# Optimization experiments

Measured on AMD Instinct MI355X. Metric: run time of the kernel, lower is better.

The kernel has to match this reference:

```python
import jax, jax.numpy as jnp
import numpy as np


def setup_inputs() -> dict:
    key = jax.random.key(0)
    ks = jax.random.split(key, 12)
    B, Nv, C, H, W = 4, 4096, 64, 376, 1240
    inp = {
        "voxel_features": jax.random.normal(ks[0], (B, Nv, C), jnp.float32),
        "voxels_3d": jax.random.normal(ks[1], (B, Nv, 3), jnp.float32),
        "img_feats": jax.random.normal(ks[2], (B, C, H, W), jnp.float32),
        "vox_x": jax.random.randint(ks[3], (B, Nv), 0, 1400, jnp.int32),
        "vox_y": jax.random.randint(ks[4], (B, Nv), 0, 430, jnp.int32),
        "q_w": jax.random.normal(ks[5], (C, C), jnp.float32) / np.sqrt(C),
        "q_b": jnp.zeros((C,), jnp.float32),
        "k_w": jax.random.normal(ks[6], (C, 3), jnp.float32) / np.sqrt(3.0),
        "k_b": jnp.zeros((C,), jnp.float32),
        "v_w": jax.random.normal(ks[7], (C, C), jnp.float32) / np.sqrt(C),
        "v_b": jnp.zeros((C,), jnp.float32),
        "o_w": jax.random.normal(ks[8], (C, C), jnp.float32) / np.sqrt(C),
        "o_b": jnp.zeros((C,), jnp.float32),
        "fc_w": jax.random.normal(ks[9], (C, C), jnp.float32) / np.sqrt(C),
    }
    return inp


def reference(voxel_features, voxels_3d, img_feats, vox_x, vox_y,
              q_w, q_b, k_w, k_b, v_w, v_b, o_w, o_b, fc_w):
    # voxel_features: [B, Nv, C] lidar voxel features (value)
    # voxels_3d:      [B, Nv, 3] voxel 3D coords (key)
    # img_feats:      [B, C, H, W] image feature map
    B, C, H, W = img_feats.shape
    Nv = voxel_features.shape[1]

    # --- gather image features at projected voxel pixel coords, zero if OOB ---
    valid = (vox_x >= 0) & (vox_x < W) & (vox_y >= 0) & (vox_y < H)  # [B, Nv]
    xc = jnp.clip(vox_x, 0, W - 1)
    yc = jnp.clip(vox_y, 0, H - 1)
    b_idx = jnp.arange(B)[:, None]
    camera = img_feats[b_idx, :, yc, xc]            # [B, Nv, C]
    camera = jnp.where(valid[..., None], camera, 0.0)

    # --- single-head cross-modal attention (q=camera, k=coords, v=lidar) ---
    scale = 1.0 / jnp.sqrt(jnp.asarray(C, camera.dtype))
    q = (camera @ q_w.T + q_b) * scale              # [B, Nv, C]
    k = voxels_3d @ k_w.T + k_b                     # [B, Nv, C]
    v = voxel_features @ v_w.T + v_b                # [B, Nv, C]
    scores = jnp.einsum('bqc,bkc->bqk', q, k)       # [B, Nv, Nv]
    attn = jax.nn.softmax(scores, axis=-1)
    ctx = jnp.einsum('bqk,bkc->bqc', attn, v)
    ctx = ctx @ o_w.T + o_b                         # out_proj

    fused = jax.nn.relu(ctx @ fc_w.T)               # [B, Nv, C]
    return jnp.concatenate([voxel_features, fused], axis=-1)  # [B, Nv, 2C]
```

## Files before the change

kernel.cpp:

```cpp
#include <hip/hip_runtime.h>

#define BB 4
#define NV 4096
#define BN (BB * NV)
#define CC 64
#define HH 376
#define WW 1240
#define HW (HH * WW)
#define LDT 72
#define LDK 36
#define NSPLIT 4
#define TILES 16
#define QSCALE 0.1803368801111244f

typedef __bf16 bf16x8 __attribute__((ext_vector_type(8)));
typedef __bf16 bf16x4 __attribute__((ext_vector_type(4)));
typedef float  f32x4  __attribute__((ext_vector_type(4)));

__global__ __launch_bounds__(256) void kprep(
    const float* __restrict__ vfeat, const float* __restrict__ v3d,
    const float* __restrict__ img, const int* __restrict__ vx,
    const int* __restrict__ vy, const float* __restrict__ qw,
    const float* __restrict__ qb, const float* __restrict__ kwm,
    const float* __restrict__ vw, const float* __restrict__ vb,
    float* __restrict__ out, unsigned short* __restrict__ Qp,
    unsigned short* __restrict__ K32, unsigned short* __restrict__ VTb) {
  __shared__ float VfS[32][68];
  __shared__ float CamS[32][68];
  __shared__ float WqkS[64][4];
  __shared__ float bqkS[4];
  const int tid = threadIdx.x;
  const int vl = tid >> 3;
  const int p = tid & 7;
  const int gv = blockIdx.x * 32 + vl;
  const int b = gv >> 12, n = gv & (NV - 1);
  const size_t row = (size_t)b * NV + n;

  if (tid < 192) {
    int j = tid / 3, d = tid - j * 3;
    float a = 0.f;
    for (int c = 0; c < CC; ++c) a = fmaf(qw[c * CC + j], kwm[c * 3 + d], a);
    WqkS[j][d] = a;
  } else if (tid < 195) {
    int d = tid - 192;
    float a = 0.f;
    for (int c = 0; c < CC; ++c) a = fmaf(qb[c], kwm[c * 3 + d], a);
    bqkS[d] = a;
  }

  {
    const float4* vf4 = (const float4*)(vfeat + row * CC) + p * 2;
    float4* o4 = (float4*)(out + row * 128) + p * 2;
    float4* s4 = (float4*)&VfS[vl][p * 8];
#pragma unroll
    for (int i = 0; i < 2; ++i) { float4 t = vf4[i]; o4[i] = t; s4[i] = t; }
  }

  {
    int x = vx[row], y = vy[row];
    bool valid = (x >= 0) & (x < WW) & (y >= 0) & (y < HH);
    int xs = valid ? x : 0, ys = valid ? y : 0;
    const float* ib = img + ((size_t)b * CC + p * 8) * (size_t)HW + (size_t)ys * WW + xs;
#pragma unroll
    for (int i = 0; i < 8; ++i) {
      float cv = ib[(size_t)i * HW];
      CamS[vl][p * 8 + i] = valid ? cv : 0.f;
    }
  }

  if (p == 0) {
    float c0 = v3d[row * 3 + 0], c1 = v3d[row * 3 + 1], c2 = v3d[row * 3 + 2];
    bf16x8 kp = {(__bf16)c0, (__bf16)c1, (__bf16)c2, (__bf16)0.f,
                 (__bf16)0.f, (__bf16)0.f, (__bf16)0.f, (__bf16)0.f};
    *(bf16x8*)(K32 + row * 32) = kp;
  } else if (p < 4) {
    bf16x8 z = {(__bf16)0.f, (__bf16)0.f, (__bf16)0.f, (__bf16)0.f,
                (__bf16)0.f, (__bf16)0.f, (__bf16)0.f, (__bf16)0.f};
    *(bf16x8*)(K32 + row * 32 + p * 8) = z;
  }
  __syncthreads();

  {
    f32x4 vr[16];
#pragma unroll
    for (int i = 0; i < 16; ++i) vr[i] = *(const f32x4*)&VfS[vl][i * 4];
#pragma unroll
    for (int cc = 0; cc < 8; ++cc) {
      int c = p * 8 + cc;
      const float4* w4 = (const float4*)(vw + c * CC);
      float acc = vb[c];
#pragma unroll
      for (int j = 0; j < 16; ++j) {
        float4 w = w4[j];
        acc = fmaf(vr[j][0], w.x, fmaf(vr[j][1], w.y, fmaf(vr[j][2], w.z, fmaf(vr[j][3], w.w, acc))));
      }
      ((__bf16*)VTb)[((size_t)b * CC + c) * NV + n] = (__bf16)acc;
    }
  }

  if (p == 0) {
    float q0 = bqkS[0], q1 = bqkS[1], q2 = bqkS[2];
#pragma unroll 8
    for (int j = 0; j < CC; ++j) {
      float c = CamS[vl][j];
      q0 = fmaf(c, WqkS[j][0], q0);
      q1 = fmaf(c, WqkS[j][1], q1);
      q2 = fmaf(c, WqkS[j][2], q2);
    }
    bf16x8 qp = {(__bf16)(q0 * QSCALE), (__bf16)(q1 * QSCALE), (__bf16)(q2 * QSCALE),
                 (__bf16)0.f, (__bf16)0.f, (__bf16)0.f, (__bf16)0.f, (__bf16)0.f};
    *(bf16x8*)(Qp + row * 32) = qp;
  } else if (p < 4) {
    bf16x8 z = {(__bf16)0.f, (__bf16)0.f, (__bf16)0.f, (__bf16)0.f,
                (__bf16)0.f, (__bf16)0.f, (__bf16)0.f, (__bf16)0.f};
    *(bf16x8*)(Qp + row * 32 + p * 8) = z;
  }
}

__global__ __launch_bounds__(256, 4) void kattn(const unsigned short* __restrict__ Qp,
                                                const unsigned short* __restrict__ K32,
                                                const unsigned short* __restrict__ VTb,
                                                unsigned short* __restrict__ Opb,
                                                float* __restrict__ ml) {
  __shared__ unsigned short Ks[2][64 * LDK];
  __shared__ unsigned short Vs[2][64 * LDT];
  __shared__ unsigned short Ps[4][16 * LDT];

  const int bid = blockIdx.x;
  const int xcd = bid & 7;
  const int idx = bid >> 3;
  const int combo = xcd * 2 + (idx >> 6);
  const int qc = idx & 63;
  const int b = combo >> 2;
  const int sp = combo & 3;
  const int q0 = qc * 64;
  const int key0 = sp * (TILES * 64);

  const int tid = threadIdx.x;
  const int wid = tid >> 6;
  const int lane = tid & 63;
  const int lq = lane & 15;
  const int lg = lane >> 4;

  const int srow = tid >> 2;
  const int scol = (tid & 3) * 16;
  const int kcol = (tid & 3) * 8;

  bf16x8 qf = *(const bf16x8*)(Qp + ((size_t)b * NV + q0 + wid * 16 + lq) * 32 + lg * 8);

  const f32x4 cinit = {-16.f, -16.f, -16.f, -16.f};
  float l_run = 0.f;
  f32x4 oacc[4];
#pragma unroll
  for (int t = 0; t < 4; ++t) oacc[t] = {0.f, 0.f, 0.f, 0.f};

  const unsigned short* kgb = K32 + ((size_t)b * NV) * 32;
  const unsigned short* vgb = VTb + (size_t)b * CC * NV;

  uint4 kq, vr0, vr1;
  {
    kq = *(const uint4*)(kgb + (size_t)(key0 + srow) * 32 + kcol);
    const uint4* vsrc = (const uint4*)(vgb + (size_t)srow * NV + key0 + scol);
    vr0 = vsrc[0]; vr1 = vsrc[1];
    *(uint4*)&Ks[0][srow * LDK + kcol] = kq;
    uint4* vdst = (uint4*)&Vs[0][srow * LDT + scol];
    vdst[0] = vr0; vdst[1] = vr1;
  }
  __syncthreads();

  int cur = 0;
  for (int tt = 0; tt < TILES; ++tt) {
    if (tt + 1 < TILES) {
      int k0 = key0 + (tt + 1) * 64;
      kq = *(const uint4*)(kgb + (size_t)(k0 + srow) * 32 + kcol);
      const uint4* vsrc = (const uint4*)(vgb + (size_t)srow * NV + k0 + scol);
      vr0 = vsrc[0]; vr1 = vsrc[1];
    }

    f32x4 s[4];
#pragma unroll
    for (int t = 0; t < 4; ++t) {
      bf16x8 ka = *(const bf16x8*)&Ks[cur][(t * 16 + lq) * LDK + lg * 8];
      s[t] = __builtin_amdgcn_mfma_f32_16x16x32_bf16(ka, qf, cinit, 0, 0, 0);
    }

#pragma unroll
    for (int t = 0; t < 4; ++t) {
      float p0 = __builtin_amdgcn_exp2f(s[t][0]);
      float p1 = __builtin_amdgcn_exp2f(s[t][1]);
      float p2 = __builtin_amdgcn_exp2f(s[t][2]);
      float p3 = __builtin_amdgcn_exp2f(s[t][3]);
      l_run += (p0 + p1) + (p2 + p3);
      bf16x4 pk;
      pk[0] = (__bf16)p0; pk[1] = (__bf16)p1; pk[2] = (__bf16)p2; pk[3] = (__bf16)p3;
      *(bf16x4*)&Ps[wid][lq * LDT + t * 16 + lg * 4] = pk;
    }

#pragma unroll
    for (int ks = 0; ks < 2; ++ks) {
      bf16x8 pa = *(const bf16x8*)&Ps[wid][lq * LDT + ks * 32 + lg * 8];
#pragma unroll
      for (int t = 0; t < 4; ++t) {
        bf16x8 vbf = *(const bf16x8*)&Vs[cur][(t * 16 + lq) * LDT + ks * 32 + lg * 8];
        oacc[t] = __builtin_amdgcn_mfma_f32_16x16x32_bf16(pa, vbf, oacc[t], 0, 0, 0);
      }
    }

    if (tt + 1 < TILES) {
      *(uint4*)&Ks[cur ^ 1][srow * LDK + kcol] = kq;
      uint4* vdst = (uint4*)&Vs[cur ^ 1][srow * LDT + scol];
      vdst[0] = vr0; vdst[1] = vr1;
    }
    __syncthreads();
    cur ^= 1;
  }

  l_run += __shfl_xor(l_run, 16);
  l_run += __shfl_xor(l_run, 32);

  const size_t obase = (size_t)sp * BN + (size_t)b * NV + q0 + wid * 16;
#pragma unroll
  for (int r = 0; r < 4; ++r) {
    __bf16* op = (__bf16*)Opb + (obase + lg * 4 + r) * CC + lq;
#pragma unroll
    for (int t = 0; t < 4; ++t) op[t * 16] = (__bf16)oacc[t][r];
  }
  if (lg == 0) ml[obase + lq] = l_run;
}

__global__ __launch_bounds__(256) void kmerge(const unsigned short* __restrict__ Opb,
                                              const float* __restrict__ ml,
                                              const float* __restrict__ ow,
                                              const float* __restrict__ ob,
                                              const float* __restrict__ fc,
                                              float* __restrict__ out) {
  __shared__ unsigned short W2s[64 * LDT];
  __shared__ float b2s[64];
  const int tid = threadIdx.x;
  const int wid = tid >> 6;
  const int lane = tid & 63;
  const int lq = lane & 15;
  const int lg = lane >> 4;

  {
    const int i = tid >> 2;
    const int jb = (tid & 3) * 16;
    float acc[16];
#pragma unroll
    for (int e = 0; e < 16; ++e) acc[e] = 0.f;
    for (int k = 0; k < CC; ++k) {
      float f = fc[i * CC + k];
      const float4* o4 = (const float4*)(ow + k * CC + jb);
#pragma unroll
      for (int e4 = 0; e4 < 4; ++e4) {
        float4 o = o4[e4];
        acc[e4 * 4 + 0] = fmaf(f, o.x, acc[e4 * 4 + 0]);
        acc[e4 * 4 + 1] = fmaf(f, o.y, acc[e4 * 4 + 1]);
        acc[e4 * 4 + 2] = fmaf(f, o.z, acc[e4 * 4 + 2]);
        acc[e4 * 4 + 3] = fmaf(f, o.w, acc[e4 * 4 + 3]);
      }
    }
    __bf16* wrow = (__bf16*)&W2s[i * LDT + jb];
#pragma unroll
    for (int e = 0; e < 16; ++e) wrow[e] = (__bf16)acc[e];
    if (tid < CC) {
      float a = 0.f;
      for (int k = 0; k < CC; ++k) a = fmaf(fc[tid * CC + k], ob[k], a);
      b2s[tid] = a;
    }
  }
  __syncthreads();

  const int row = blockIdx.x * 64 + wid * 16 + lq;

  float lstar = 0.f;
#pragma unroll
  for (int s = 0; s < NSPLIT; ++s) lstar += ml[(size_t)s * BN + row];

  float ctx[16];
#pragma unroll
  for (int j = 0; j < 16; ++j) ctx[j] = 0.f;
#pragma unroll
  for (int s = 0; s < NSPLIT; ++s) {
    const __bf16* oprow = (const __bf16*)Opb + ((size_t)s * BN + row) * CC;
    bf16x8 a0 = *(const bf16x8*)(oprow + lg * 8);
    bf16x8 a1 = *(const bf16x8*)(oprow + 32 + lg * 8);
#pragma unroll
    for (int j = 0; j < 8; ++j) {
      ctx[j] += (float)a0[j];
      ctx[8 + j] += (float)a1[j];
    }
  }
  float inv = 1.f / lstar;
  bf16x8 cb0, cb1;
#pragma unroll
  for (int j = 0; j < 8; ++j) {
    cb0[j] = (__bf16)(ctx[j] * inv);
    cb1[j] = (__bf16)(ctx[8 + j] * inv);
  }

  const f32x4 vzero = {0.f, 0.f, 0.f, 0.f};
  float* orow = out + (size_t)row * 128 + 64;
#pragma unroll
  for (int t2 = 0; t2 < 4; ++t2) {
    bf16x8 wa0 = *(const bf16x8*)&W2s[(t2 * 16 + lq) * LDT + lg * 8];
    bf16x8 wa1 = *(const bf16x8*)&W2s[(t2 * 16 + lq) * LDT + 32 + lg * 8];
    f32x4 r2 = vzero;
    r2 = __builtin_amdgcn_mfma_f32_16x16x32_bf16(wa0, cb0, r2, 0, 0, 0);
    r2 = __builtin_amdgcn_mfma_f32_16x16x32_bf16(wa1, cb1, r2, 0, 0, 0);
    float4 o;
    o.x = fmaxf(r2[0] + b2s[t2 * 16 + lg * 4 + 0], 0.f);
    o.y = fmaxf(r2[1] + b2s[t2 * 16 + lg * 4 + 1], 0.f);
    o.z = fmaxf(r2[2] + b2s[t2 * 16 + lg * 4 + 2], 0.f);
    o.w = fmaxf(r2[3] + b2s[t2 * 16 + lg * 4 + 3], 0.f);
    *(float4*)(orow + t2 * 16 + lg * 4) = o;
  }
}

extern "C" void kernel_launch(void* const* d_in, const int* in_sizes, int n_in,
                              void* d_out, int out_size, void* d_ws, size_t ws_size,
                              hipStream_t stream) {
  const float* vfeat = (const float*)d_in[0];
  const float* v3d = (const float*)d_in[1];
  const float* img = (const float*)d_in[2];
  const int* vx = (const int*)d_in[3];
  const int* vy = (const int*)d_in[4];
  const float* qw = (const float*)d_in[5];
  const float* qb = (const float*)d_in[6];
  const float* kwm = (const float*)d_in[7];
  const float* vw = (const float*)d_in[9];
  const float* vb = (const float*)d_in[10];
  const float* ow = (const float*)d_in[11];
  const float* ob = (const float*)d_in[12];
  const float* fc = (const float*)d_in[13];
  float* out = (float*)d_out;

  char* ws = (char*)d_ws;
  unsigned short* Qp = (unsigned short*)(ws);
  unsigned short* K32 = (unsigned short*)(ws + (1u << 20));
  unsigned short* VTb = (unsigned short*)(ws + (2u << 20));
  unsigned short* Opb = (unsigned short*)(ws + (4u << 20));
  float* ml = (float*)(ws + (12u << 20));

  kprep<<<512, 256, 0, stream>>>(vfeat, v3d, img, vx, vy, qw, qb, kwm, vw, vb,
                                 out, Qp, K32, VTb);
  kattn<<<1024, 256, 0, stream>>>(Qp, K32, VTb, Opb, ml);
  kmerge<<<256, 256, 0, stream>>>(Opb, ml, ow, ob, fc, out);
}
```

Baseline: 101.0 us.

## Process two query sub-tiles per wave in attention kernel to reuse K/V tiles

Each wave now handles 32 query rows (two 16-row MFMA sub-tiles) instead of 16, so every block covers 128 queries and the grid halves to 512 blocks. Each K and V tile loaded into shared memory and read from LDS is reused for twice the MFMA work, which cuts global and LDS traffic per query. In exchange, accumulator registers double, launch bounds drop to 2 blocks per CU, and fewer blocks are available to fill the device.

```diff
diff --git a/kernel.cpp b/kernel.cpp
--- a/kernel.cpp
+++ b/kernel.cpp
@@ -117,23 +117,23 @@
   }
 }
 
-__global__ __launch_bounds__(256, 4) void kattn(const unsigned short* __restrict__ Qp,
+__global__ __launch_bounds__(256, 2) void kattn(const unsigned short* __restrict__ Qp,
                                                 const unsigned short* __restrict__ K32,
                                                 const unsigned short* __restrict__ VTb,
                                                 unsigned short* __restrict__ Opb,
                                                 float* __restrict__ ml) {
   __shared__ unsigned short Ks[2][64 * LDK];
   __shared__ unsigned short Vs[2][64 * LDT];
-  __shared__ unsigned short Ps[4][16 * LDT];
+  __shared__ unsigned short Ps[4][2][16 * LDT];
 
   const int bid = blockIdx.x;
   const int xcd = bid & 7;
   const int idx = bid >> 3;
-  const int combo = xcd * 2 + (idx >> 6);
-  const int qc = idx & 63;
+  const int combo = xcd * 2 + (idx >> 5);
+  const int qc = idx & 31;
   const int b = combo >> 2;
   const int sp = combo & 3;
-  const int q0 = qc * 64;
+  const int q0 = qc * 128;
   const int key0 = sp * (TILES * 64);
 
   const int tid = threadIdx.x;
@@ -146,13 +146,15 @@
   const int scol = (tid & 3) * 16;
   const int kcol = (tid & 3) * 8;
 
-  bf16x8 qf = *(const bf16x8*)(Qp + ((size_t)b * NV + q0 + wid * 16 + lq) * 32 + lg * 8);
+  const size_t qrow = (size_t)b * NV + q0 + wid * 32 + lq;
+  bf16x8 qf0 = *(const bf16x8*)(Qp + qrow * 32 + lg * 8);
+  bf16x8 qf1 = *(const bf16x8*)(Qp + (qrow + 16) * 32 + lg * 8);
 
   const f32x4 cinit = {-16.f, -16.f, -16.f, -16.f};
-  float l_run = 0.f;
-  f32x4 oacc[4];
-#pragma unroll
-  for (int t = 0; t < 4; ++t) oacc[t] = {0.f, 0.f, 0.f, 0.f};
+  float l0 = 0.f, l1 = 0.f;
+  f32x4 oacc0[4], oacc1[4];
+#pragma unroll
+  for (int t = 0; t < 4; ++t) { oacc0[t] = {0.f, 0.f, 0.f, 0.f}; oacc1[t] = {0.f, 0.f, 0.f, 0.f}; }
 
   const unsigned short* kgb = K32 + ((size_t)b * NV) * 32;
   const unsigned short* vgb = VTb + (size_t)b * CC * NV;
@@ -177,32 +179,43 @@
       vr0 = vsrc[0]; vr1 = vsrc[1];
     }
 
-    f32x4 s[4];
+    f32x4 s0[4], s1[4];
 #pragma unroll
     for (int t = 0; t < 4; ++t) {
       bf16x8 ka = *(const bf16x8*)&Ks[cur][(t * 16 + lq) * LDK + lg * 8];
-      s[t] = __builtin_amdgcn_mfma_f32_16x16x32_bf16(ka, qf, cinit, 0, 0, 0);
+      s0[t] = __builtin_amdgcn_mfma_f32_16x16x32_bf16(ka, qf0, cinit, 0, 0, 0);
+      s1[t] = __builtin_amdgcn_mfma_f32_16x16x32_bf16(ka, qf1, cinit, 0, 0, 0);
     }
 
 #pragma unroll
     for (int t = 0; t < 4; ++t) {
-      float p0 = __builtin_amdgcn_exp2f(s[t][0]);
-      float p1 = __builtin_amdgcn_exp2f(s[t][1]);
-      float p2 = __builtin_amdgcn_exp2f(s[t][2]);
-      float p3 = __builtin_amdgcn_exp2f(s[t][3]);
-      l_run += (p0 + p1) + (p2 + p3);
-      bf16x4 pk;
-      pk[0] = (__bf16)p0; pk[1] = (__bf16)p1; pk[2] = (__bf16)p2; pk[3] = (__bf16)p3;
-      *(bf16x4*)&Ps[wid][lq * LDT + t * 16 + lg * 4] = pk;
+      float a0 = __builtin_amdgcn_exp2f(s0[t][0]);
+      float a1 = __builtin_amdgcn_exp2f(s0[t][1]);
+      float a2 = __builtin_amdgcn_exp2f(s0[t][2]);
+      float a3 = __builtin_amdgcn_exp2f(s0[t][3]);
+      l0 += (a0 + a1) + (a2 + a3);
+      bf16x4 pk0;
+      pk0[0] = (__bf16)a0; pk0[1] = (__bf16)a1; pk0[2] = (__bf16)a2; pk0[3] = (__bf16)a3;
+      *(bf16x4*)&Ps[wid][0][lq * LDT + t * 16 + lg * 4] = pk0;
+      float c0 = __builtin_amdgcn_exp2f(s1[t][0]);
+      float c1 = __builtin_amdgcn_exp2f(s1[t][1]);
+      float c2 = __builtin_amdgcn_exp2f(s1[t][2]);
+      float c3 = __builtin_amdgcn_exp2f(s1[t][3]);
+      l1 += (c0 + c1) + (c2 + c3);
+      bf16x4 pk1;
+      pk1[0] = (__bf16)c0; pk1[1] = (__bf16)c1; pk1[2] = (__bf16)c2; pk1[3] = (__bf16)c3;
+      *(bf16x4*)&Ps[wid][1][lq * LDT + t * 16 + lg * 4] = pk1;
     }
 
 #pragma unroll
     for (int ks = 0; ks < 2; ++ks) {
-      bf16x8 pa = *(const bf16x8*)&Ps[wid][lq * LDT + ks * 32 + lg * 8];
+      bf16x8 pa0 = *(const bf16x8*)&Ps[wid][0][lq * LDT + ks * 32 + lg * 8];
+      bf16x8 pa1 = *(const bf16x8*)&Ps[wid][1][lq * LDT + ks * 32 + lg * 8];
 #pragma unroll
       for (int t = 0; t < 4; ++t) {
         bf16x8 vbf = *(const bf16x8*)&Vs[cur][(t * 16 + lq) * LDT + ks * 32 + lg * 8];
-        oacc[t] = __builtin_amdgcn_mfma_f32_16x16x32_bf16(pa, vbf, oacc[t], 0, 0, 0);
+        oacc0[t] = __builtin_amdgcn_mfma_f32_16x16x32_bf16(pa0, vbf, oacc0[t], 0, 0, 0);
+        oacc1[t] = __builtin_amdgcn_mfma_f32_16x16x32_bf16(pa1, vbf, oacc1[t], 0, 0, 0);
       }
     }
 
@@ -215,17 +228,24 @@
     cur ^= 1;
   }
 
-  l_run += __shfl_xor(l_run, 16);
-  l_run += __shfl_xor(l_run, 32);
-
-  const size_t obase = (size_t)sp * BN + (size_t)b * NV + q0 + wid * 16;
+  l0 += __shfl_xor(l0, 16); l0 += __shfl_xor(l0, 32);
+  l1 += __shfl_xor(l1, 16); l1 += __shfl_xor(l1, 32);
+
+  const size_t obase = (size_t)sp * BN + (size_t)b * NV + q0 + wid * 32;
 #pragma unroll
   for (int r = 0; r < 4; ++r) {
-    __bf16* op = (__bf16*)Opb + (obase + lg * 4 + r) * CC + lq;
-#pragma unroll
-    for (int t = 0; t < 4; ++t) op[t * 16] = (__bf16)oacc[t][r];
-  }
-  if (lg == 0) ml[obase + lq] = l_run;
+    __bf16* op0 = (__bf16*)Opb + (obase + lg * 4 + r) * CC + lq;
+    __bf16* op1 = (__bf16*)Opb + (obase + 16 + lg * 4 + r) * CC + lq;
+#pragma unroll
+    for (int t = 0; t < 4; ++t) {
+      op0[t * 16] = (__bf16)oacc0[t][r];
+      op1[t * 16] = (__bf16)oacc1[t][r];
+    }
+  }
+  if (lg == 0) {
+    ml[obase + lq] = l0;
+    ml[obase + 16 + lq] = l1;
+  }
 }
 
 __global__ __launch_bounds__(256) void kmerge(const unsigned short* __restrict__ Opb,
@@ -344,6 +364,6 @@
 
   kprep<<<512, 256, 0, stream>>>(vfeat, v3d, img, vx, vy, qw, qb, kwm, vw, vb,
                                  out, Qp, K32, VTb);
-  kattn<<<1024, 256, 0, stream>>>(Qp, K32, VTb, Opb, ml);
+  kattn<<<512, 256, 0, stream>>>(Qp, K32, VTb, Opb, ml);
   kmerge<<<256, 256, 0, stream>>>(Opb, ml, ow, ob, fc, out);
 }
```

New measurement: 98.24 us. 1.03x faster.
